# Optimization experiments

Measured on AMD Instinct MI355X. Metric: run time of the kernel, lower is better.

The kernel has to match this reference:

```python
import jax, jax.numpy as jnp
import numpy as np
from jax import lax

B, N, C_IN, H, W = 256, 64, 3, 8, 8
CH = [32, 64, 128]   # cnn channels per stage
D = 128              # fc / gnn width
OUT = 5
BN_EPS = 1e-5


def setup_inputs() -> dict:
    key = jax.random.key(0)
    ks = jax.random.split(key, 24)
    x = jax.random.normal(ks[0], (B, N, C_IN, H, W), jnp.float32)
    # sparse symmetric communication graph, no self loops (GCNConv adds them)
    a = jax.random.uniform(ks[1], (B, N, N)) < 0.15
    a = jnp.logical_or(a, jnp.swapaxes(a, 1, 2)).astype(jnp.float32)
    gso = a * (1.0 - jnp.eye(N, dtype=jnp.float32))

    def lin(k, o, i):
        return (jax.random.normal(k, (o, i), jnp.float32) / np.sqrt(i)).astype(jnp.float32)

    def conv(k, o, i):
        return (jax.random.normal(k, (o, i, 3, 3), jnp.float32) / np.sqrt(i * 9)).astype(jnp.float32)

    inp = {
        'x': x, 'gso': gso,
        'w_c1': conv(ks[2], CH[0], C_IN), 'b_c1': jnp.zeros((CH[0],), jnp.float32),
        'g_bn1': jnp.ones((CH[0],), jnp.float32), 'be_bn1': jnp.zeros((CH[0],), jnp.float32),
        'w_c2': conv(ks[3], CH[1], CH[0]), 'b_c2': jnp.zeros((CH[1],), jnp.float32),
        'g_bn2': jnp.ones((CH[1],), jnp.float32), 'be_bn2': jnp.zeros((CH[1],), jnp.float32),
        'w_c3': conv(ks[4], CH[2], CH[1]), 'b_c3': jnp.zeros((CH[2],), jnp.float32),
        'g_bn3': jnp.ones((CH[2],), jnp.float32), 'be_bn3': jnp.zeros((CH[2],), jnp.float32),
        'w_fc': lin(ks[5], D, CH[2]), 'b_fc': jnp.zeros((D,), jnp.float32),
        'w_g1': lin(ks[6], D, D), 'b_g1': jnp.zeros((D,), jnp.float32),
        'w_g2': lin(ks[7], D, D), 'b_g2': jnp.zeros((D,), jnp.float32),
        'w_out': lin(ks[8], OUT, D), 'b_out': jnp.zeros((OUT,), jnp.float32),
    }
    return inp


def _cnn_block(h, w, b, g, be):
    h = lax.conv_general_dilated(h, w, (1, 1), 'SAME',
                                 dimension_numbers=('NCHW', 'OIHW', 'NCHW'))
    h = h + b[None, :, None, None]
    # eval-mode BatchNorm2d with running_mean=0, running_var=1
    h = h * (g / jnp.sqrt(1.0 + BN_EPS))[None, :, None, None] + be[None, :, None, None]
    h = jax.nn.relu(h)
    h = lax.reduce_window(h, -jnp.inf, lax.max, (1, 1, 2, 2), (1, 1, 2, 2), 'VALID')
    return h


def _forward(x, gso, w_c1, b_c1, g_bn1, be_bn1, w_c2, b_c2, g_bn2, be_bn2,
             w_c3, b_c3, g_bn3, be_bn3, w_fc, b_fc, w_g1, b_g1, w_g2, b_g2,
             w_out, b_out):
    b, n = x.shape[0], x.shape[1]
    h = x.reshape(b * n, x.shape[2], x.shape[3], x.shape[4])  # vectorize agents
    h = _cnn_block(h, w_c1, b_c1, g_bn1, be_bn1)
    h = _cnn_block(h, w_c2, b_c2, g_bn2, be_bn2)
    h = _cnn_block(h, w_c3, b_c3, g_bn3, be_bn3)          # [B*N, CH2, 1, 1]
    h = h.reshape(b * n, -1)
    h = jax.nn.relu(h @ w_fc.T + b_fc)                    # [B*N, D]
    feat = h.reshape(b, n, -1)
    # GCNConv: add self loops (weight 1), symmetric normalization
    a1 = gso + jnp.eye(n, dtype=gso.dtype)
    dinv = lax.rsqrt(a1.sum(-1))                          # deg >= 1
    ahat = dinv[:, :, None] * a1 * dinv[:, None, :]       # [B, N, N]
    hg = jax.nn.relu(jnp.einsum('bij,bjf->bif', ahat, feat @ w_g1.T) + b_g1)
    hg = jax.nn.relu(jnp.einsum('bij,bjf->bif', ahat, hg @ w_g2.T) + b_g2)
    actions = hg @ w_out.T + b_out                        # [B, N, OUT]
    return actions


def reference(x, gso, w_c1, b_c1, g_bn1, be_bn1, w_c2, b_c2, g_bn2, be_bn2,
              w_c3, b_c3, g_bn3, be_bn3, w_fc, b_fc, w_g1, b_g1, w_g2, b_g2,
              w_out, b_out):
    return _forward(x, gso, w_c1, b_c1, g_bn1, be_bn1, w_c2, b_c2, g_bn2, be_bn2,
                    w_c3, b_c3, g_bn3, be_bn3, w_fc, b_fc, w_g1, b_g1, w_g2, b_g2,
                    w_out, b_out)
```

## Files before the change

kernel.cpp:

```cpp
#include <hip/hip_runtime.h>
#include <math.h>


typedef __attribute__((ext_vector_type(8))) short bf16x8;
typedef __attribute__((ext_vector_type(4))) float f32x4;

__device__ __forceinline__ short f2bf(float f) {
  union { float f; unsigned u; } v; v.f = f;
  unsigned r = v.u + 0x7fffu + ((v.u >> 16) & 1u);
  return (short)(r >> 16);
}
__device__ __forceinline__ float bf2f(unsigned short u) {
  union { unsigned u; float f; } v; v.u = ((unsigned)u) << 16;
  return v.f;
}

__global__ __launch_bounds__(256) void pack_all(
    const float* __restrict__ w_c1, const float* __restrict__ w_c2,
    const float* __restrict__ w_c3, const float* __restrict__ w_fc,
    const float* __restrict__ w_g1, const float* __restrict__ w_g2,
    short* __restrict__ B1, short* __restrict__ B2, short* __restrict__ B3,
    short* __restrict__ Wfc, short* __restrict__ Wg1, short* __restrict__ Wg2) {
  int idx = blockIdx.x * 256 + threadIdx.x;
  if (idx < 2048) {
    int oc = idx >> 6, k = idx & 63;
    int t = k >> 2, ic = k & 3;
    float v = (t < 9 && ic < 3) ? w_c1[(oc * 3 + ic) * 9 + t] : 0.0f;
    B1[idx] = f2bf(v);
  } else if (idx < 20480) {
    int i2 = idx - 2048;
    int oc = i2 / 288, r = i2 - oc * 288;
    int t = r >> 5, ic = r & 31;
    B2[i2] = f2bf(w_c2[(oc * 32 + ic) * 9 + t]);
  } else if (idx < 94208) {
    int i3 = idx - 20480;
    int oc = i3 / 576, r = i3 - oc * 576;
    int t = r >> 6, ic = r & 63;
    B3[i3] = f2bf(w_c3[(oc * 64 + ic) * 9 + t]);
  } else if (idx < 110592) {
    int i = idx - 94208; Wfc[i] = f2bf(w_fc[i]);
  } else if (idx < 126976) {
    int i = idx - 110592; Wg1[i] = f2bf(w_g1[i]);
  } else if (idx < 143360) {
    int i = idx - 126976; Wg2[i] = f2bf(w_g2[i]);
  }
}

__global__ __launch_bounds__(256, 2) void conv_all(
    const float* __restrict__ x, const short* __restrict__ B1g,
    const short* __restrict__ B2g, const short* __restrict__ B3g,
    const float* __restrict__ b1, const float* __restrict__ g1,
    const float* __restrict__ e1, const float* __restrict__ b2,
    const float* __restrict__ g2, const float* __restrict__ e2,
    const float* __restrict__ b3, const float* __restrict__ g3,
    const float* __restrict__ e3, short* __restrict__ c3) {
  __shared__ short sMix[16 * 584];
  __shared__ short sc1[16 * 640];
  __shared__ short sc2[16 * 296];
  const int tid = threadIdx.x;
  const int s0 = blockIdx.x * 16;
  const int lane = tid & 63, w = tid >> 6;
  const int col = lane & 15, quad = lane >> 4;
  const int m = lane & 15;

  for (int i = tid; i < 800; i += 256)
    *(uint4*)(sMix + i * 8) = (uint4){0, 0, 0, 0};
  __syncthreads();
#pragma unroll
  for (int it = 0; it < 4; ++it) {
    int p = it * 256 + tid;
    int si = p >> 6, pix = p & 63;
    int y = pix >> 3, xx2 = pix & 7;
    const float* xb = x + (s0 + si) * 192 + pix;
    ushort4 o;
    o.x = (unsigned short)f2bf(xb[0]);
    o.y = (unsigned short)f2bf(xb[64]);
    o.z = (unsigned short)f2bf(xb[128]);
    o.w = 0;
    *(ushort4*)(sMix + si * 400 + ((y + 1) * 10 + xx2 + 1) * 4) = o;
  }
  __syncthreads();

  {
    bf16x8 Bf[2][2];
#pragma unroll
    for (int nt = 0; nt < 2; ++nt)
#pragma unroll
      for (int ks = 0; ks < 2; ++ks)
        Bf[nt][ks] = *(const bf16x8*)(B1g + (nt * 16 + col) * 64 + ks * 32 + quad * 8);
    float Abn[2], Cbn[2];
#pragma unroll
    for (int nt = 0; nt < 2; ++nt) {
      int oc = nt * 16 + col;
      float a = g1[oc] * rsqrtf(1.0f + 1e-5f);
      Abn[nt] = a;
      Cbn[nt] = fmaf(b1[oc], a, e1[oc]);
    }
    const int t0 = 2 * quad, t1 = t0 + 1;
    const int ky0 = t0 / 3, kx0 = t0 - 3 * (t0 / 3);
    const int ky1 = t1 / 3, kx1 = t1 - 3 * (t1 / 3);
    const int pl = m >> 2, sub = m & 3;
    const int dy = sub >> 1, dx = sub & 1;
    const uint2 z2 = {0u, 0u};
#pragma unroll
    for (int sl = 0; sl < 4; ++sl) {
      const int si = w * 4 + sl;
      const short* xb = sMix + si * 400;
#pragma unroll
      for (int tile = 0; tile < 4; ++tile) {
        const int pi = tile * 4 + pl;
        const int py = pi >> 2, px = pi & 3;
        const int cy = 2 * py + dy, cx = 2 * px + dx;
        union { bf16x8 v; uint2 u[2]; } a0, a1;
        a0.u[0] = *(const uint2*)(xb + ((cy + ky0) * 10 + cx + kx0) * 4);
        a0.u[1] = *(const uint2*)(xb + ((cy + ky1) * 10 + cx + kx1) * 4);
        uint2 u8 = *(const uint2*)(xb + ((cy + 2) * 10 + cx + 2) * 4);
        a1.u[0] = (quad == 0) ? u8 : z2;
        a1.u[1] = z2;
        f32x4 acc0 = {0, 0, 0, 0}, acc1 = {0, 0, 0, 0};
        acc0 = __builtin_amdgcn_mfma_f32_16x16x32_bf16(a0.v, Bf[0][0], acc0, 0, 0, 0);
        acc0 = __builtin_amdgcn_mfma_f32_16x16x32_bf16(a1.v, Bf[0][1], acc0, 0, 0, 0);
        acc1 = __builtin_amdgcn_mfma_f32_16x16x32_bf16(a0.v, Bf[1][0], acc1, 0, 0, 0);
        acc1 = __builtin_amdgcn_mfma_f32_16x16x32_bf16(a1.v, Bf[1][1], acc1, 0, 0, 0);
        const int piq = tile * 4 + quad;
#pragma unroll
        for (int nt = 0; nt < 2; ++nt) {
          f32x4 acc = nt ? acc1 : acc0;
          float p0 = fmaf(acc[0], Abn[nt], Cbn[nt]);
          float p1 = fmaf(acc[1], Abn[nt], Cbn[nt]);
          float p2 = fmaf(acc[2], Abn[nt], Cbn[nt]);
          float p3 = fmaf(acc[3], Abn[nt], Cbn[nt]);
          float mx = fmaxf(fmaxf(fmaxf(p0, p1), fmaxf(p2, p3)), 0.0f);
          sc1[si * 640 + piq * 40 + nt * 16 + col] = f2bf(mx);
        }
      }
    }
  }
  __syncthreads();

  {
    bf16x8 Bf[4][9];
#pragma unroll
    for (int nt = 0; nt < 4; ++nt)
#pragma unroll
      for (int t = 0; t < 9; ++t)
        Bf[nt][t] = *(const bf16x8*)(B2g + (nt * 16 + col) * 288 + t * 32 + quad * 8);
    float Abn[4], Cbn[4];
#pragma unroll
    for (int nt = 0; nt < 4; ++nt) {
      int oc = nt * 16 + col;
      float a = g2[oc] * rsqrtf(1.0f + 1e-5f);
      Abn[nt] = a;
      Cbn[nt] = fmaf(b2[oc], a, e2[oc]);
    }
    const int q2 = m >> 2, sub = m & 3;
    const int cy = 2 * (q2 >> 1) + (sub >> 1);
    const int cx = 2 * (q2 & 1) + (sub & 1);
    int off[9];
    bool valid[9];
#pragma unroll
    for (int t = 0; t < 9; ++t) {
      int ky = t / 3, kx = t - 3 * (t / 3);
      int yy = cy + ky - 1, xx = cx + kx - 1;
      valid[t] = ((unsigned)yy < 4u) && ((unsigned)xx < 4u);
      int yc = min(max(yy, 0), 3), xc = min(max(xx, 0), 3);
      off[t] = (yc * 4 + xc) * 40 + quad * 8;
    }
    const bf16x8 zf = {0, 0, 0, 0, 0, 0, 0, 0};
#pragma unroll
    for (int sl = 0; sl < 4; ++sl) {
      const int si = w * 4 + sl;
      const short* ib = sc1 + si * 640;
      f32x4 acc[4];
#pragma unroll
      for (int nt = 0; nt < 4; ++nt) acc[nt] = (f32x4){0, 0, 0, 0};
#pragma unroll
      for (int t = 0; t < 9; ++t) {
        bf16x8 a = *(const bf16x8*)(ib + off[t]);
        if (!valid[t]) a = zf;
#pragma unroll
        for (int nt = 0; nt < 4; ++nt)
          acc[nt] = __builtin_amdgcn_mfma_f32_16x16x32_bf16(a, Bf[nt][t], acc[nt], 0, 0, 0);
      }
#pragma unroll
      for (int nt = 0; nt < 4; ++nt) {
        float p0 = fmaf(acc[nt][0], Abn[nt], Cbn[nt]);
        float p1 = fmaf(acc[nt][1], Abn[nt], Cbn[nt]);
        float p2 = fmaf(acc[nt][2], Abn[nt], Cbn[nt]);
        float p3 = fmaf(acc[nt][3], Abn[nt], Cbn[nt]);
        float mx = fmaxf(fmaxf(fmaxf(p0, p1), fmaxf(p2, p3)), 0.0f);
        sc2[si * 296 + quad * 72 + nt * 16 + col] = f2bf(mx);
      }
    }
  }
  __syncthreads();

  {
    const int cp = m & 3, sl3 = m >> 2;
    const int cy = cp >> 1, cx = cp & 1;
    const short* ib = sc2 + (w * 4 + sl3) * 296;
    bf16x8 A[18];
    const bf16x8 zf = {0, 0, 0, 0, 0, 0, 0, 0};
#pragma unroll
    for (int ks = 0; ks < 18; ++ks) {
      int t = ks >> 1;
      int ky = t / 3, kx = t - 3 * (t / 3);
      int iy = cy + ky - 1, ix = cx + kx - 1;
      bool valid = ((unsigned)iy < 2u) && ((unsigned)ix < 2u);
      int iyc = min(max(iy, 0), 1), ixc = min(max(ix, 0), 1);
      bf16x8 a = *(const bf16x8*)(ib + (iyc * 2 + ixc) * 72 + (ks & 1) * 32 + quad * 8);
      A[ks] = valid ? a : zf;
    }
    f32x4 acc[8];
#pragma unroll
    for (int i = 0; i < 8; ++i) acc[i] = (f32x4){0, 0, 0, 0};
#pragma unroll 1
    for (int ng = 0; ng < 8; ++ng) {
      __syncthreads();
      for (int c = tid; c < 1152; c += 256) {
        int row = c / 72, seg = c - row * 72;
        *(bf16x8*)(sMix + row * 584 + seg * 8) =
            *(const bf16x8*)(B3g + (ng * 16 + row) * 576 + seg * 8);
      }
      __syncthreads();
      const int nB = col * 584 + quad * 8;
#pragma unroll
      for (int ks = 0; ks < 18; ++ks) {
        bf16x8 b = *(const bf16x8*)(sMix + nB + ks * 32);
        acc[ng] = __builtin_amdgcn_mfma_f32_16x16x32_bf16(A[ks], b, acc[ng], 0, 0, 0);
      }
    }
    const int sample = s0 + w * 4 + quad;
#pragma unroll
    for (int ng = 0; ng < 8; ++ng) {
      int oc = ng * 16 + col;
      float a = g3[oc] * rsqrtf(1.0f + 1e-5f);
      float cc = fmaf(b3[oc], a, e3[oc]);
      float p0 = fmaf(acc[ng][0], a, cc);
      float p1 = fmaf(acc[ng][1], a, cc);
      float p2 = fmaf(acc[ng][2], a, cc);
      float p3 = fmaf(acc[ng][3], a, cc);
      float mx = fmaxf(fmaxf(fmaxf(p0, p1), fmaxf(p2, p3)), 0.0f);
      c3[sample * 128 + oc] = f2bf(mx);
    }
  }
}

__global__ __launch_bounds__(512) void fused_dense(
    const short* __restrict__ c3, const float* __restrict__ gso,
    const short* __restrict__ Wfc, const short* __restrict__ Wg1,
    const short* __restrict__ Wg2, const float* __restrict__ b_fc,
    const float* __restrict__ b_g1, const float* __restrict__ b_g2,
    const float* __restrict__ w_o, const float* __restrict__ b_o,
    float* __restrict__ out) {
  __shared__ short sAct[64 * 136];
  __shared__ short sT[128 * 72];
  __shared__ short sAhat[64 * 72];
  __shared__ float sDinv[64];
  __shared__ float sWo[640];
  const int tid = threadIdx.x;
  const int b = blockIdx.x;
  float* sG = (float*)sT;
  for (int i = tid; i < 4096; i += 512) sG[i] = gso[b * 4096 + i];
  for (int i = tid; i < 640; i += 512) sWo[i] = w_o[i];
  __syncthreads();
  if (tid < 64) {
    float ssum = 1.0f;
    for (int j = 0; j < 64; ++j) ssum += sG[j * 64 + tid];
    sDinv[tid] = rsqrtf(ssum);
  }
  __syncthreads();
  for (int i = tid; i < 4096; i += 512) {
    int r = i >> 6, c = i & 63;
    float v = sDinv[r] * (sG[i] + (r == c ? 1.0f : 0.0f)) * sDinv[c];
    sAhat[r * 72 + c] = f2bf(v);
  }
  for (int i = tid; i < 1024; i += 512) {
    int r = i >> 4, seg = i & 15;
    *(bf16x8*)(sAct + r * 136 + seg * 8) =
        *(const bf16x8*)(c3 + (b * 64 + r) * 128 + seg * 8);
  }
  __syncthreads();
  const int lane = tid & 63, w8 = tid >> 6;
  const int rg = w8 >> 1, nh = w8 & 1;
  const int col = lane & 15, quad = lane >> 4;
  const int arow = (rg * 16 + col) * 136;
  const int crow0 = (rg * 16 + quad * 4) * 136;
  bf16x8 A[4];
  f32x4 acc[4];

#pragma unroll
  for (int ks = 0; ks < 4; ++ks)
    A[ks] = *(const bf16x8*)(sAct + arow + ks * 32 + quad * 8);
  __syncthreads();
#pragma unroll
  for (int i = 0; i < 4; ++i) acc[i] = (f32x4){0, 0, 0, 0};
#pragma unroll
  for (int ntl = 0; ntl < 4; ++ntl) {
    const int n = (nh * 4 + ntl) * 16 + col;
#pragma unroll
    for (int ks = 0; ks < 4; ++ks) {
      bf16x8 bb = *(const bf16x8*)(Wfc + n * 128 + ks * 32 + quad * 8);
      acc[ntl] = __builtin_amdgcn_mfma_f32_16x16x32_bf16(A[ks], bb, acc[ntl], 0, 0, 0);
    }
  }
#pragma unroll
  for (int ntl = 0; ntl < 4; ++ntl) {
    const int n = (nh * 4 + ntl) * 16 + col;
    const float bv = b_fc[n];
#pragma unroll
    for (int reg = 0; reg < 4; ++reg)
      sAct[crow0 + reg * 136 + n] = f2bf(fmaxf(acc[ntl][reg] + bv, 0.0f));
  }
  __syncthreads();

#pragma unroll
  for (int ks = 0; ks < 4; ++ks)
    A[ks] = *(const bf16x8*)(sAct + arow + ks * 32 + quad * 8);
#pragma unroll
  for (int i = 0; i < 4; ++i) acc[i] = (f32x4){0, 0, 0, 0};
#pragma unroll
  for (int ntl = 0; ntl < 4; ++ntl) {
    const int n = (nh * 4 + ntl) * 16 + col;
#pragma unroll
    for (int ks = 0; ks < 4; ++ks) {
      bf16x8 bb = *(const bf16x8*)(Wg1 + n * 128 + ks * 32 + quad * 8);
      acc[ntl] = __builtin_amdgcn_mfma_f32_16x16x32_bf16(A[ks], bb, acc[ntl], 0, 0, 0);
    }
  }
#pragma unroll
  for (int ntl = 0; ntl < 4; ++ntl) {
    const int n = (nh * 4 + ntl) * 16 + col;
    ushort4 pk;
    pk.x = (unsigned short)f2bf(acc[ntl][0]);
    pk.y = (unsigned short)f2bf(acc[ntl][1]);
    pk.z = (unsigned short)f2bf(acc[ntl][2]);
    pk.w = (unsigned short)f2bf(acc[ntl][3]);
    *(ushort4*)(sT + n * 72 + rg * 16 + quad * 4) = pk;
  }
  __syncthreads();

  bf16x8 Ah[2];
#pragma unroll
  for (int ks = 0; ks < 2; ++ks)
    Ah[ks] = *(const bf16x8*)(sAhat + (rg * 16 + col) * 72 + ks * 32 + quad * 8);
#pragma unroll
  for (int i = 0; i < 4; ++i) acc[i] = (f32x4){0, 0, 0, 0};
#pragma unroll
  for (int ntl = 0; ntl < 4; ++ntl) {
    const int n = (nh * 4 + ntl) * 16 + col;
#pragma unroll
    for (int ks = 0; ks < 2; ++ks) {
      bf16x8 bb = *(const bf16x8*)(sT + n * 72 + ks * 32 + quad * 8);
      acc[ntl] = __builtin_amdgcn_mfma_f32_16x16x32_bf16(Ah[ks], bb, acc[ntl], 0, 0, 0);
    }
  }
#pragma unroll
  for (int ntl = 0; ntl < 4; ++ntl) {
    const int n = (nh * 4 + ntl) * 16 + col;
    const float bv = b_g1[n];
#pragma unroll
    for (int reg = 0; reg < 4; ++reg)
      sAct[crow0 + reg * 136 + n] = f2bf(fmaxf(acc[ntl][reg] + bv, 0.0f));
  }
  __syncthreads();

#pragma unroll
  for (int ks = 0; ks < 4; ++ks)
    A[ks] = *(const bf16x8*)(sAct + arow + ks * 32 + quad * 8);
#pragma unroll
  for (int i = 0; i < 4; ++i) acc[i] = (f32x4){0, 0, 0, 0};
#pragma unroll
  for (int ntl = 0; ntl < 4; ++ntl) {
    const int n = (nh * 4 + ntl) * 16 + col;
#pragma unroll
    for (int ks = 0; ks < 4; ++ks) {
      bf16x8 bb = *(const bf16x8*)(Wg2 + n * 128 + ks * 32 + quad * 8);
      acc[ntl] = __builtin_amdgcn_mfma_f32_16x16x32_bf16(A[ks], bb, acc[ntl], 0, 0, 0);
    }
  }
#pragma unroll
  for (int ntl = 0; ntl < 4; ++ntl) {
    const int n = (nh * 4 + ntl) * 16 + col;
    ushort4 pk;
    pk.x = (unsigned short)f2bf(acc[ntl][0]);
    pk.y = (unsigned short)f2bf(acc[ntl][1]);
    pk.z = (unsigned short)f2bf(acc[ntl][2]);
    pk.w = (unsigned short)f2bf(acc[ntl][3]);
    *(ushort4*)(sT + n * 72 + rg * 16 + quad * 4) = pk;
  }
  __syncthreads();

#pragma unroll
  for (int i = 0; i < 4; ++i) acc[i] = (f32x4){0, 0, 0, 0};
#pragma unroll
  for (int ntl = 0; ntl < 4; ++ntl) {
    const int n = (nh * 4 + ntl) * 16 + col;
#pragma unroll
    for (int ks = 0; ks < 2; ++ks) {
      bf16x8 bb = *(const bf16x8*)(sT + n * 72 + ks * 32 + quad * 8);
      acc[ntl] = __builtin_amdgcn_mfma_f32_16x16x32_bf16(Ah[ks], bb, acc[ntl], 0, 0, 0);
    }
  }
#pragma unroll
  for (int ntl = 0; ntl < 4; ++ntl) {
    const int n = (nh * 4 + ntl) * 16 + col;
    const float bv = b_g2[n];
#pragma unroll
    for (int reg = 0; reg < 4; ++reg)
      sAct[crow0 + reg * 136 + n] = f2bf(fmaxf(acc[ntl][reg] + bv, 0.0f));
  }
  __syncthreads();

  if (tid < 320) {
    const int j = tid / 5, o = tid - 5 * j;
    float a0 = 0.0f;
#pragma unroll
    for (int k8 = 0; k8 < 16; ++k8) {
      union { bf16x8 v; unsigned short u[8]; } h;
      h.v = *(const bf16x8*)(sAct + j * 136 + k8 * 8);
#pragma unroll
      for (int jj = 0; jj < 8; ++jj)
        a0 = fmaf(bf2f(h.u[jj]), sWo[o * 128 + k8 * 8 + jj], a0);
    }
    out[(b * 64 + j) * 5 + o] = a0 + b_o[o];
  }
}

extern "C" void kernel_launch(void* const* d_in, const int* in_sizes, int n_in,
                              void* d_out, int out_size, void* d_ws, size_t ws_size,
                              hipStream_t stream) {
  const float* x    = (const float*)d_in[0];
  const float* gso  = (const float*)d_in[1];
  const float* w_c1 = (const float*)d_in[2];
  const float* b_c1 = (const float*)d_in[3];
  const float* g_b1 = (const float*)d_in[4];
  const float* e_b1 = (const float*)d_in[5];
  const float* w_c2 = (const float*)d_in[6];
  const float* b_c2 = (const float*)d_in[7];
  const float* g_b2 = (const float*)d_in[8];
  const float* e_b2 = (const float*)d_in[9];
  const float* w_c3 = (const float*)d_in[10];
  const float* b_c3 = (const float*)d_in[11];
  const float* g_b3 = (const float*)d_in[12];
  const float* e_b3 = (const float*)d_in[13];
  const float* w_fc = (const float*)d_in[14];
  const float* b_fc = (const float*)d_in[15];
  const float* w_g1 = (const float*)d_in[16];
  const float* b_g1 = (const float*)d_in[17];
  const float* w_g2 = (const float*)d_in[18];
  const float* b_g2 = (const float*)d_in[19];
  const float* w_o  = (const float*)d_in[20];
  const float* b_o  = (const float*)d_in[21];
  float* out = (float*)d_out;
  char* ws = (char*)d_ws;

  short* c3  = (short*)(ws + 0);
  short* B1  = (short*)(ws + 4194304);
  short* B2  = (short*)(ws + 4198400);
  short* B3  = (short*)(ws + 4235264);
  short* Wfc = (short*)(ws + 4382720);
  short* Wg1 = (short*)(ws + 4415488);
  short* Wg2 = (short*)(ws + 4448256);

  pack_all<<<560, 256, 0, stream>>>(w_c1, w_c2, w_c3, w_fc, w_g1, w_g2,
                                    B1, B2, B3, Wfc, Wg1, Wg2);
  conv_all<<<1024, 256, 0, stream>>>(x, B1, B2, B3, b_c1, g_b1, e_b1,
                                     b_c2, g_b2, e_b2, b_c3, g_b3, e_b3, c3);
  fused_dense<<<256, 512, 0, stream>>>(c3, gso, Wfc, Wg1, Wg2, b_fc, b_g1,
                                       b_g2, w_o, b_o, out);
}
```

Before: 177.1 us.

## Pre-pack conv weights in MFMA fragment order and read stage-3 B from global

The weight packing kernel now writes conv weights in per-lane MFMA fragment order, so each lane loads its B operand with one contiguous 16-byte load and a wave's loads are fully coalesced. Stage 3 no longer stages B3 tiles through shared memory with two block barriers per output group; it reads fragments directly from global/L2 and fully unrolls the loop. Shared buffers are shrunk by removing padding. The exchange is more global load traffic and register pressure, and the unpadded LDS strides may bring back bank conflicts.

```diff
diff --git a/kernel.cpp b/kernel.cpp
--- a/kernel.cpp
+++ b/kernel.cpp
@@ -23,19 +23,29 @@
     short* __restrict__ Wfc, short* __restrict__ Wg1, short* __restrict__ Wg2) {
   int idx = blockIdx.x * 256 + threadIdx.x;
   if (idx < 2048) {
-    int oc = idx >> 6, k = idx & 63;
+    int j = idx & 7, lane = (idx >> 3) & 63, f = idx >> 9;
+    int nt = f >> 1, ksp = f & 1;
+    int col = lane & 15, quad = lane >> 4;
+    int k = ksp * 32 + quad * 8 + j;
     int t = k >> 2, ic = k & 3;
+    int oc = nt * 16 + col;
     float v = (t < 9 && ic < 3) ? w_c1[(oc * 3 + ic) * 9 + t] : 0.0f;
     B1[idx] = f2bf(v);
   } else if (idx < 20480) {
     int i2 = idx - 2048;
-    int oc = i2 / 288, r = i2 - oc * 288;
-    int t = r >> 5, ic = r & 31;
+    int j = i2 & 7, lane = (i2 >> 3) & 63, f = i2 >> 9;
+    int nt = f / 9, t = f - nt * 9;
+    int col = lane & 15, quad = lane >> 4;
+    int oc = nt * 16 + col, ic = quad * 8 + j;
     B2[i2] = f2bf(w_c2[(oc * 32 + ic) * 9 + t]);
   } else if (idx < 94208) {
     int i3 = idx - 20480;
-    int oc = i3 / 576, r = i3 - oc * 576;
-    int t = r >> 6, ic = r & 63;
+    int j = i3 & 7, lane = (i3 >> 3) & 63, f = i3 >> 9;
+    int ng = f / 18, ks = f - ng * 18;
+    int col = lane & 15, quad = lane >> 4;
+    int oc = ng * 16 + col;
+    int k = ks * 32 + quad * 8 + j;
+    int t = k >> 6, ic = k & 63;
     B3[i3] = f2bf(w_c3[(oc * 64 + ic) * 9 + t]);
   } else if (idx < 110592) {
     int i = idx - 94208; Wfc[i] = f2bf(w_fc[i]);
@@ -47,16 +57,16 @@
 }
 
 __global__ __launch_bounds__(256, 2) void conv_all(
-    const float* __restrict__ x, const short* __restrict__ B1g,
-    const short* __restrict__ B2g, const short* __restrict__ B3g,
+    const float* __restrict__ x, const short* __restrict__ B1f,
+    const short* __restrict__ B2f, const short* __restrict__ B3f,
     const float* __restrict__ b1, const float* __restrict__ g1,
     const float* __restrict__ e1, const float* __restrict__ b2,
     const float* __restrict__ g2, const float* __restrict__ e2,
     const float* __restrict__ b3, const float* __restrict__ g3,
     const float* __restrict__ e3, short* __restrict__ c3) {
-  __shared__ short sMix[16 * 584];
-  __shared__ short sc1[16 * 640];
-  __shared__ short sc2[16 * 296];
+  __shared__ short sFrame[16 * 400];
+  __shared__ short sc1[16 * 512];
+  __shared__ short sc2[16 * 256];
   const int tid = threadIdx.x;
   const int s0 = blockIdx.x * 16;
   const int lane = tid & 63, w = tid >> 6;
@@ -64,7 +74,7 @@
   const int m = lane & 15;
 
   for (int i = tid; i < 800; i += 256)
-    *(uint4*)(sMix + i * 8) = (uint4){0, 0, 0, 0};
+    *(uint4*)(sFrame + i * 8) = (uint4){0, 0, 0, 0};
   __syncthreads();
 #pragma unroll
   for (int it = 0; it < 4; ++it) {
@@ -77,7 +87,7 @@
     o.y = (unsigned short)f2bf(xb[64]);
     o.z = (unsigned short)f2bf(xb[128]);
     o.w = 0;
-    *(ushort4*)(sMix + si * 400 + ((y + 1) * 10 + xx2 + 1) * 4) = o;
+    *(ushort4*)(sFrame + si * 400 + ((y + 1) * 10 + xx2 + 1) * 4) = o;
   }
   __syncthreads();
 
@@ -87,7 +97,7 @@
     for (int nt = 0; nt < 2; ++nt)
 #pragma unroll
       for (int ks = 0; ks < 2; ++ks)
-        Bf[nt][ks] = *(const bf16x8*)(B1g + (nt * 16 + col) * 64 + ks * 32 + quad * 8);
+        Bf[nt][ks] = *(const bf16x8*)(B1f + ((nt * 2 + ks) << 9) + lane * 8);
     float Abn[2], Cbn[2];
 #pragma unroll
     for (int nt = 0; nt < 2; ++nt) {
@@ -105,7 +115,7 @@
 #pragma unroll
     for (int sl = 0; sl < 4; ++sl) {
       const int si = w * 4 + sl;
-      const short* xb = sMix + si * 400;
+      const short* xb = sFrame + si * 400;
 #pragma unroll
       for (int tile = 0; tile < 4; ++tile) {
         const int pi = tile * 4 + pl;
@@ -131,7 +141,7 @@
           float p2 = fmaf(acc[2], Abn[nt], Cbn[nt]);
           float p3 = fmaf(acc[3], Abn[nt], Cbn[nt]);
           float mx = fmaxf(fmaxf(fmaxf(p0, p1), fmaxf(p2, p3)), 0.0f);
-          sc1[si * 640 + piq * 40 + nt * 16 + col] = f2bf(mx);
+          sc1[si * 512 + piq * 32 + nt * 16 + col] = f2bf(mx);
         }
       }
     }
@@ -144,7 +154,7 @@
     for (int nt = 0; nt < 4; ++nt)
 #pragma unroll
       for (int t = 0; t < 9; ++t)
-        Bf[nt][t] = *(const bf16x8*)(B2g + (nt * 16 + col) * 288 + t * 32 + quad * 8);
+        Bf[nt][t] = *(const bf16x8*)(B2f + ((nt * 9 + t) << 9) + lane * 8);
     float Abn[4], Cbn[4];
 #pragma unroll
     for (int nt = 0; nt < 4; ++nt) {
@@ -164,13 +174,13 @@
       int yy = cy + ky - 1, xx = cx + kx - 1;
       valid[t] = ((unsigned)yy < 4u) && ((unsigned)xx < 4u);
       int yc = min(max(yy, 0), 3), xc = min(max(xx, 0), 3);
-      off[t] = (yc * 4 + xc) * 40 + quad * 8;
+      off[t] = (yc * 4 + xc) * 32 + quad * 8;
     }
     const bf16x8 zf = {0, 0, 0, 0, 0, 0, 0, 0};
 #pragma unroll
     for (int sl = 0; sl < 4; ++sl) {
       const int si = w * 4 + sl;
-      const short* ib = sc1 + si * 640;
+      const short* ib = sc1 + si * 512;
       f32x4 acc[4];
 #pragma unroll
       for (int nt = 0; nt < 4; ++nt) acc[nt] = (f32x4){0, 0, 0, 0};
@@ -189,7 +199,7 @@
         float p2 = fmaf(acc[nt][2], Abn[nt], Cbn[nt]);
         float p3 = fmaf(acc[nt][3], Abn[nt], Cbn[nt]);
         float mx = fmaxf(fmaxf(fmaxf(p0, p1), fmaxf(p2, p3)), 0.0f);
-        sc2[si * 296 + quad * 72 + nt * 16 + col] = f2bf(mx);
+        sc2[si * 256 + quad * 64 + nt * 16 + col] = f2bf(mx);
       }
     }
   }
@@ -198,7 +208,7 @@
   {
     const int cp = m & 3, sl3 = m >> 2;
     const int cy = cp >> 1, cx = cp & 1;
-    const short* ib = sc2 + (w * 4 + sl3) * 296;
+    const short* ib = sc2 + (w * 4 + sl3) * 256;
     bf16x8 A[18];
     const bf16x8 zf = {0, 0, 0, 0, 0, 0, 0, 0};
 #pragma unroll
@@ -208,25 +218,17 @@
       int iy = cy + ky - 1, ix = cx + kx - 1;
       bool valid = ((unsigned)iy < 2u) && ((unsigned)ix < 2u);
       int iyc = min(max(iy, 0), 1), ixc = min(max(ix, 0), 1);
-      bf16x8 a = *(const bf16x8*)(ib + (iyc * 2 + ixc) * 72 + (ks & 1) * 32 + quad * 8);
+      bf16x8 a = *(const bf16x8*)(ib + (iyc * 2 + ixc) * 64 + (ks & 1) * 32 + quad * 8);
       A[ks] = valid ? a : zf;
     }
     f32x4 acc[8];
 #pragma unroll
     for (int i = 0; i < 8; ++i) acc[i] = (f32x4){0, 0, 0, 0};
-#pragma unroll 1
+#pragma unroll
     for (int ng = 0; ng < 8; ++ng) {
-      __syncthreads();
-      for (int c = tid; c < 1152; c += 256) {
-        int row = c / 72, seg = c - row * 72;
-        *(bf16x8*)(sMix + row * 584 + seg * 8) =
-            *(const bf16x8*)(B3g + (ng * 16 + row) * 576 + seg * 8);
-      }
-      __syncthreads();
-      const int nB = col * 584 + quad * 8;
 #pragma unroll
       for (int ks = 0; ks < 18; ++ks) {
-        bf16x8 b = *(const bf16x8*)(sMix + nB + ks * 32);
+        bf16x8 b = *(const bf16x8*)(B3f + (((ng * 18 + ks) << 6) + lane) * 8);
         acc[ng] = __builtin_amdgcn_mfma_f32_16x16x32_bf16(A[ks], b, acc[ng], 0, 0, 0);
       }
     }
```

Measured after the change: 156.8 us, median of 2. 1.13x faster.
